# Kernel tuning notes

Measured on AMD Instinct MI355X. Metric: run time of the kernel, lower is better.

The kernel has to match this reference:

```python
import math
import jax, jax.numpy as jnp
import numpy as np

KERNEL_SIZES = [3, 5, 7, 9, 11, 13, 15, 17]
NUM_HEADS = 2
EMBED = len(KERNEL_SIZES)  # 8
HEAD_DIM = EMBED // NUM_HEADS  # 4


def _moving_avg(x2, k):
    # x2: [B, S]; replicate-pad so output length == S (MovingAvg padding scheme)
    front = k - 1 - (k - 1) // 2
    end = (k - 1) // 2
    p = jnp.concatenate([
        jnp.repeat(x2[:, :1], front, axis=1), x2,
        jnp.repeat(x2[:, -1:], end, axis=1)
    ], axis=1)  # [B, S+k-1]
    w = jnp.full((1, 1, k), 1.0 / k, dtype=x2.dtype)
    y = jax.lax.conv_general_dilated(p[:, None, :], w, (1,), 'VALID')
    return y[:, 0, :]  # [B, S]


def setup_inputs() -> dict:
    key = jax.random.key(0)
    ks = jax.random.split(key, 6)
    B, S = 32, 2048
    D, E = HEAD_DIM, EMBED
    sd = 1.0 / math.sqrt(D)
    x = jax.random.normal(ks[0], (B, S, 1), dtype=jnp.float32)
    Wq = jax.random.normal(ks[1], (D, D), dtype=jnp.float32) * sd
    Wk = jax.random.normal(ks[2], (D, D), dtype=jnp.float32) * sd
    Wv = jax.random.normal(ks[3], (D, D), dtype=jnp.float32) * sd
    Wo = jax.random.normal(ks[4], (E, E), dtype=jnp.float32) * (1.0 / math.sqrt(E))
    bo = jax.random.normal(ks[5], (E,), dtype=jnp.float32) * 0.01
    return {"x": x, "Wq": Wq, "Wk": Wk, "Wv": Wv, "Wo": Wo, "bo": bo}


def reference(x, Wq, Wk, Wv, Wo, bo):
    B, S, _ = x.shape
    H, D, E = NUM_HEADS, HEAD_DIM, EMBED
    x2 = x[..., 0]  # [B, S]
    # multi moving-average branches -> concat on channel dim
    mm = jnp.stack([_moving_avg(x2, k) for k in KERNEL_SIZES], axis=-1)  # [B,S,E]
    t = mm.reshape(B, S, H, D)
    # nn.Linear(head_dim, head_dim, bias=False): y = x @ W^T (shared across heads)
    q = jnp.einsum('bshd,ed->bshe', t, Wq)
    k_ = jnp.einsum('bshd,ed->bshe', t, Wk)
    v = jnp.einsum('bshd,ed->bshe', t, Wv)
    scale = jnp.asarray(math.sqrt(D), dtype=x.dtype)
    energy = jnp.einsum('bqhd,bkhd->bhqk', q, k_) / scale  # [B,H,S,S]
    att = jax.nn.softmax(energy, axis=-1)  # dropout is identity in eval mode
    o = jnp.einsum('bhqk,bkhd->bqhd', att, v).reshape(B, S, E)
    o = o @ Wo.T + bo  # fc_out
    weights = jax.nn.softmax(o, axis=-1)  # [B,S,E]
    trend = jnp.sum(mm * weights, axis=-1, keepdims=True)  # [B,S,1]
    seasonal = x - trend
    return seasonal, trend
```

## Files before the change

kernel.cpp:

```cpp
#include <hip/hip_runtime.h>

#define SB 32
#define SS 2048
#define SH 2
#define SD 4
#define SE 8

#define LOG2E 1.44269504f

typedef float    f32x16 __attribute__((ext_vector_type(16)));
typedef _Float16 f16x8  __attribute__((ext_vector_type(8)));

static __device__ __forceinline__ float fast_exp2(float x) {
#if __has_builtin(__builtin_amdgcn_exp2f)
    return __builtin_amdgcn_exp2f(x);
#else
    return exp2f(x);
#endif
}

static __device__ __forceinline__ int cvtpk(float a, float b) {
    auto h = __builtin_amdgcn_cvt_pkrtz(a, b);
    union { decltype(h) hh; int i; } u; u.hh = h; return u.i;
}

static __device__ __forceinline__ void swap32(int a, int b, int lane, int& r0, int& r1) {
#if __has_builtin(__builtin_amdgcn_permlane32_swap)
    auto r = __builtin_amdgcn_permlane32_swap(a, b, false, false);
    r0 = r[0]; r1 = r[1];
#else
    const int blo = __builtin_amdgcn_ds_bpermute((lane & 31) << 2, b);
    const int ahi = __builtin_amdgcn_ds_bpermute(((lane ^ 32) & 63) << 2, a);
    r0 = (lane < 32) ? a : blo;
    r1 = (lane < 32) ? ahi : b;
#endif
}

static __device__ __forceinline__ f16x8 frag2(unsigned x, unsigned y) {
    union { unsigned u[4]; f16x8 h; } c;
    c.u[0] = x; c.u[1] = y; c.u[2] = 0; c.u[3] = 0; return c.h;
}
static __device__ __forceinline__ f16x8 frag4(uint4 v) {
    union { uint4 u; f16x8 h; } c; c.u = v; return c.h;
}
static __device__ __forceinline__ f16x8 fragi(int a, int b, int c_, int d) {
    union { int u[4]; f16x8 h; } c;
    c.u[0] = a; c.u[1] = b; c.u[2] = c_; c.u[3] = d; return c.h;
}

union u32h2 { unsigned u; _Float16 h[2]; };
static __device__ __forceinline__ unsigned packh2(float a, float b) {
    u32h2 c; c.h[0] = (_Float16)a; c.h[1] = (_Float16)b; return c.u;
}

__global__ __launch_bounds__(256) void k_ma_qkv(
    const float* __restrict__ x,
    const float* __restrict__ Wq,
    const float* __restrict__ Wk,
    const float* __restrict__ Wv,
    uint2* __restrict__ qws16,
    uint2* __restrict__ kws16,
    _Float16* __restrict__ vtg,
    float4* __restrict__ mmws)
{
    __shared__ float xs[272];

    const int tile = blockIdx.x % (SS / 256);
    const int b    = blockIdx.x / (SS / 256);
    const int s0   = tile * 256;
    const float* xrow = x + b * SS;

    for (int i = threadIdx.x; i < 272; i += 256) {
        int idx = s0 - 8 + i;
        idx = min(max(idx, 0), SS - 1);
        xs[i] = xrow[idx];
    }
    __syncthreads();

    const int t = threadIdx.x;
    const int s = s0 + t;

    float mmv[8];
    float c = xs[8 + t];
    #pragma unroll
    for (int h = 1; h <= 8; ++h) {
        c += xs[8 + t - h] + xs[8 + t + h];
        mmv[h - 1] = c * (1.0f / (float)(2 * h + 1));
    }

    mmws[(b * SS + s) * 2 + 0] = make_float4(mmv[0], mmv[1], mmv[2], mmv[3]);
    mmws[(b * SS + s) * 2 + 1] = make_float4(mmv[4], mmv[5], mmv[6], mmv[7]);

    const float qscale = 0.5f * LOG2E;
    #pragma unroll
    for (int h = 0; h < SH; ++h) {
        const float t0 = mmv[h * 4 + 0];
        const float t1 = mmv[h * 4 + 1];
        const float t2 = mmv[h * 4 + 2];
        const float t3 = mmv[h * 4 + 3];
        float q[4], k[4], v[4];
        #pragma unroll
        for (int e = 0; e < 4; ++e) {
            q[e] = (t0 * Wq[e * 4 + 0] + t1 * Wq[e * 4 + 1] +
                    t2 * Wq[e * 4 + 2] + t3 * Wq[e * 4 + 3]) * qscale;
            k[e] =  t0 * Wk[e * 4 + 0] + t1 * Wk[e * 4 + 1] +
                    t2 * Wk[e * 4 + 2] + t3 * Wk[e * 4 + 3];
            v[e] =  t0 * Wv[e * 4 + 0] + t1 * Wv[e * 4 + 1] +
                    t2 * Wv[e * 4 + 2] + t3 * Wv[e * 4 + 3];
        }
        const int bh  = b * SH + h;
        const int idx = bh * SS + s;
        qws16[idx] = make_uint2(packh2(q[0], q[1]), packh2(q[2], q[3]));
        kws16[idx] = make_uint2(packh2(k[0], k[1]), packh2(k[2], k[3]));
        #pragma unroll
        for (int e = 0; e < 4; ++e)
            vtg[(bh * 4 + e) * SS + s] = (_Float16)v[e];
    }
}

#define LDS_K    0
#define LDS_VT   16384
#define VT_STRIDE 4112
#define LDS_Z    36944
#define LDS_SIZE 37376

__global__ __launch_bounds__(256) void k_attn(
    const uint2* __restrict__ qws16,
    const uint2* __restrict__ kws16,
    const unsigned* __restrict__ vtg,
    float4* __restrict__ ows)
{
    __shared__ __align__(16) char lds[LDS_SIZE];

    const int t      = threadIdx.x;
    const int bh     = blockIdx.x >> 4;
    const int w      = t >> 6;
    const int iblock = (blockIdx.x & 15) * 4 + w;
    const int lane   = t & 63;
    const int c31    = lane & 31;

    const uint2* kg = kws16 + bh * SS;
    for (int i = t; i < SS; i += 256)
        *(uint2*)(lds + LDS_K + i * 8) = kg[i];
    const unsigned* vg = vtg + bh * 4 * (SS / 2);
    for (int i = t; i < 4 * (SS / 2); i += 256) {
        const int cc = i >> 10, col = i & 1023;
        *(unsigned*)(lds + LDS_VT + cc * VT_STRIDE + col * 4) = vg[i];
    }
    for (int i = t; i < SS / 2; i += 256)
        *(unsigned*)(lds + LDS_VT + 4 * VT_STRIDE + i * 4) = 0x3C003C00u;
    if (t < 32) *(unsigned*)(lds + LDS_Z + t * 4) = 0u;
    __syncthreads();

    uint2 qq = qws16[bh * SS + iblock * 32 + c31];
    if (lane >= 32) { qq.x = 0u; qq.y = 0u; }
    const f16x8 bq = frag2(qq.x, qq.y);

    int kaddr = (lane < 32) ? (LDS_K + lane * 8) : LDS_Z;
    const int kstep = (lane < 32) ? 256 : 0;
    int vaddr = (c31 < 5) ? (LDS_VT + c31 * VT_STRIDE + (lane >> 5) * 16) : LDS_Z;
    const int vstep = (c31 < 5) ? 64 : 0;

    f32x16 oacc = {0,0,0,0,0,0,0,0,0,0,0,0,0,0,0,0};
    const f32x16 zc = {0,0,0,0,0,0,0,0,0,0,0,0,0,0,0,0};

    uint2 kk  = *(const uint2*)(lds + kaddr); kaddr += kstep;
    uint4 vv0 = *(const uint4*)(lds + vaddr);
    uint4 vv1 = *(const uint4*)(lds + vaddr + 32); vaddr += vstep;

    for (int jt = 0; jt < SS / 32; ++jt) {
        const f16x8 ak  = frag2(kk.x, kk.y);
        const f16x8 av0 = frag4(vv0);
        const f16x8 av1 = frag4(vv1);

        f32x16 d = __builtin_amdgcn_mfma_f32_32x32x16_f16(ak, bq, zc, 0, 0, 0);

        kk  = *(const uint2*)(lds + kaddr); kaddr += kstep;
        vv0 = *(const uint4*)(lds + vaddr);
        vv1 = *(const uint4*)(lds + vaddr + 32); vaddr += vstep;

        float p[16];
        #pragma unroll
        for (int r = 0; r < 16; ++r) p[r] = fast_exp2(d[r]);

        const int pk01 = cvtpk(p[0],  p[1]),  pk23 = cvtpk(p[2],  p[3]);
        const int pk45 = cvtpk(p[4],  p[5]),  pk67 = cvtpk(p[6],  p[7]);
        const int pk89 = cvtpk(p[8],  p[9]),  pkAB = cvtpk(p[10], p[11]);
        const int pkCD = cvtpk(p[12], p[13]), pkEF = cvtpk(p[14], p[15]);

        int B0, B1, B2, B3, C0, C1, C2, C3;
        swap32(pk01, pk45, lane, B0, B2);
        swap32(pk23, pk67, lane, B1, B3);
        swap32(pk89, pkCD, lane, C0, C2);
        swap32(pkAB, pkEF, lane, C1, C3);

        const f16x8 bp0 = fragi(B0, B1, B2, B3);
        const f16x8 bp1 = fragi(C0, C1, C2, C3);

        oacc = __builtin_amdgcn_mfma_f32_32x32x16_f16(av0, bp0, oacc, 0, 0, 0);
        oacc = __builtin_amdgcn_mfma_f32_32x32x16_f16(av1, bp1, oacc, 0, 0, 0);
    }

    union { float f; int i; } u0; u0.f = oacc[0];
    int s0i, s1i;
    swap32(u0.i, u0.i, lane, s0i, s1i);
    union { int i; float f; } ul; ul.i = s1i;
    if (lane < 32) {
        const float inv = 1.0f / ul.f;
        ows[bh * SS + iblock * 32 + lane] =
            make_float4(oacc[0] * inv, oacc[1] * inv, oacc[2] * inv, oacc[3] * inv);
    }
}

__global__ __launch_bounds__(256) void k_epilogue(
    const float* __restrict__ x,
    const float* __restrict__ Wo,
    const float* __restrict__ bo,
    const float4* __restrict__ ows,
    const float4* __restrict__ mmws,
    float* __restrict__ out)
{
    const int pos = blockIdx.x * 256 + threadIdx.x;
    const int b = pos / SS;
    const int s = pos % SS;

    const float4 o0 = ows[(b * SH + 0) * SS + s];
    const float4 o1 = ows[(b * SH + 1) * SS + s];
    const float ov[8] = {o0.x, o0.y, o0.z, o0.w, o1.x, o1.y, o1.z, o1.w};

    float g[8];
    float m = -1e30f;
    #pragma unroll
    for (int e = 0; e < 8; ++e) {
        float acc = bo[e];
        #pragma unroll
        for (int f = 0; f < 8; ++f) acc += ov[f] * Wo[e * 8 + f];
        g[e] = acc;
        m = fmaxf(m, acc);
    }
    float l = 0.0f;
    #pragma unroll
    for (int e = 0; e < 8; ++e) { g[e] = __expf(g[e] - m); l += g[e]; }
    const float inv = 1.0f / l;

    const float4 mm0 = mmws[pos * 2 + 0];
    const float4 mm1 = mmws[pos * 2 + 1];
    const float mv[8] = {mm0.x, mm0.y, mm0.z, mm0.w, mm1.x, mm1.y, mm1.z, mm1.w};

    float trend = 0.0f;
    #pragma unroll
    for (int e = 0; e < 8; ++e) trend += g[e] * inv * mv[e];

    out[pos]           = x[pos] - trend;
    out[SB * SS + pos] = trend;
}

extern "C" void kernel_launch(void* const* d_in, const int* in_sizes, int n_in,
                              void* d_out, int out_size, void* d_ws, size_t ws_size,
                              hipStream_t stream) {
    const float* x  = (const float*)d_in[0];
    const float* Wq = (const float*)d_in[1];
    const float* Wk = (const float*)d_in[2];
    const float* Wv = (const float*)d_in[3];
    const float* Wo = (const float*)d_in[4];
    const float* bo = (const float*)d_in[5];

    uint2*     qws16 = (uint2*)d_ws;
    uint2*     kws16 = qws16 + SB * SH * SS;
    _Float16*  vtg   = (_Float16*)(kws16 + SB * SH * SS);
    float4*    mmws  = (float4*)(vtg + SB * SH * 4 * SS);
    float4*    ows   = mmws + SB * SS * 2;

    k_ma_qkv<<<SB * (SS / 256), 256, 0, stream>>>(x, Wq, Wk, Wv, qws16, kws16, vtg, mmws);
    k_attn<<<SB * SH * 16, 256, 0, stream>>>(qws16, kws16, (const unsigned*)vtg, ows);
    k_epilogue<<<(SB * SS) / 256, 256, 0, stream>>>(x, Wo, bo, ows, mmws, (float*)d_out);
}
```

Baseline: 51.17 us.

## Split attention key dimension into two chunks and reduce partials in epilogue

The attention kernel now processes half of the key/value sequence per block, doubling the grid and halving LDS usage per block. Each block writes unnormalized partial outputs and partial row sums, and the epilogue kernel sums the chunks and normalizes. This aims to improve occupancy and CU utilization and shorten each block's serial loop. The cost is extra workspace traffic for partials and more reads in the epilogue.

```diff
diff --git a/kernel.cpp b/kernel.cpp
--- a/kernel.cpp
+++ b/kernel.cpp
@@ -5,6 +5,11 @@
 #define SH 2
 #define SD 4
 #define SE 8
+#define BHS (SB * SH * SS)
+
+#define JCH  2
+#define JLEN (SS / JCH)
+#define NT   (JLEN / 32)
 
 #define LOG2E 1.44269504f
 
@@ -118,36 +123,40 @@
     }
 }
 
-#define LDS_K    0
-#define LDS_VT   16384
-#define VT_STRIDE 4112
-#define LDS_Z    36944
-#define LDS_SIZE 37376
-
-__global__ __launch_bounds__(256) void k_attn(
+#define LDS_K     0
+#define K_BYTES   (JLEN * 8)
+#define LDS_VT    K_BYTES
+#define VT_STRIDE ((JLEN + 8) * 2)
+#define LDS_Z     (LDS_VT + 5 * VT_STRIDE)
+#define LDS_SIZE  (LDS_Z + 128)
+
+__global__ __launch_bounds__(256, 8) void k_attn(
     const uint2* __restrict__ qws16,
     const uint2* __restrict__ kws16,
     const unsigned* __restrict__ vtg,
-    float4* __restrict__ ows)
+    float4* __restrict__ pacc,
+    float* __restrict__ pl)
 {
     __shared__ __align__(16) char lds[LDS_SIZE];
 
-    const int t      = threadIdx.x;
-    const int bh     = blockIdx.x >> 4;
-    const int w      = t >> 6;
-    const int iblock = (blockIdx.x & 15) * 4 + w;
-    const int lane   = t & 63;
-    const int c31    = lane & 31;
-
-    const uint2* kg = kws16 + bh * SS;
-    for (int i = t; i < SS; i += 256)
+    const int t    = threadIdx.x;
+    const int jc   = blockIdx.x & (JCH - 1);
+    const int ig   = (blockIdx.x >> 1) & 15;
+    const int bh   = blockIdx.x >> 5;
+    const int w    = t >> 6;
+    const int iblock = ig * 4 + w;
+    const int lane = t & 63;
+    const int c31  = lane & 31;
+
+    const uint2* kg = kws16 + bh * SS + jc * JLEN;
+    for (int i = t; i < JLEN; i += 256)
         *(uint2*)(lds + LDS_K + i * 8) = kg[i];
-    const unsigned* vg = vtg + bh * 4 * (SS / 2);
-    for (int i = t; i < 4 * (SS / 2); i += 256) {
-        const int cc = i >> 10, col = i & 1023;
-        *(unsigned*)(lds + LDS_VT + cc * VT_STRIDE + col * 4) = vg[i];
-    }
-    for (int i = t; i < SS / 2; i += 256)
+    const unsigned* vg = vtg + bh * 4 * (SS / 2) + jc * (JLEN / 2);
+    for (int i = t; i < 4 * (JLEN / 2); i += 256) {
+        const int cc = i / (JLEN / 2), col = i % (JLEN / 2);
+        *(unsigned*)(lds + LDS_VT + cc * VT_STRIDE + col * 4) = vg[cc * (SS / 2) + col];
+    }
+    for (int i = t; i < JLEN / 2; i += 256)
         *(unsigned*)(lds + LDS_VT + 4 * VT_STRIDE + i * 4) = 0x3C003C00u;
     if (t < 32) *(unsigned*)(lds + LDS_Z + t * 4) = 0u;
     __syncthreads();
@@ -168,7 +177,7 @@
     uint4 vv0 = *(const uint4*)(lds + vaddr);
     uint4 vv1 = *(const uint4*)(lds + vaddr + 32); vaddr += vstep;
 
-    for (int jt = 0; jt < SS / 32; ++jt) {
+    for (int jt = 0; jt < NT; ++jt) {
         const f16x8 ak  = frag2(kk.x, kk.y);
         const f16x8 av0 = frag4(vv0);
         const f16x8 av1 = frag4(vv1);
@@ -206,9 +215,9 @@
     swap32(u0.i, u0.i, lane, s0i, s1i);
     union { int i; float f; } ul; ul.i = s1i;
     if (lane < 32) {
-        const float inv = 1.0f / ul.f;
-        ows[bh * SS + iblock * 32 + lane] =
-            make_float4(oacc[0] * inv, oacc[1] * inv, oacc[2] * inv, oacc[3] * inv);
+        const int idx = jc * BHS + bh * SS + iblock * 32 + lane;
+        pacc[idx] = make_float4(oacc[0], oacc[1], oacc[2], oacc[3]);
+        pl[idx]   = ul.f;
     }
 }
 
@@ -216,7 +225,8 @@
     const float* __restrict__ x,
     const float* __restrict__ Wo,
     const float* __restrict__ bo,
-    const float4* __restrict__ ows,
+    const float4* __restrict__ pacc,
+    const float* __restrict__ pl,
     const float4* __restrict__ mmws,
     float* __restrict__ out)
 {
@@ -224,9 +234,23 @@
     const int b = pos / SS;
     const int s = pos % SS;
 
-    const float4 o0 = ows[(b * SH + 0) * SS + s];
-    const float4 o1 = ows[(b * SH + 1) * SS + s];
-    const float ov[8] = {o0.x, o0.y, o0.z, o0.w, o1.x, o1.y, o1.z, o1.w};
+    float ov[8];
+    #pragma unroll
+    for (int h = 0; h < SH; ++h) {
+        const int base = (b * SH + h) * SS + s;
+        float lsum = 0.f, ax = 0.f, ay = 0.f, az = 0.f, aw = 0.f;
+        #pragma unroll
+        for (int jc = 0; jc < JCH; ++jc) {
+            const float4 pa = pacc[jc * BHS + base];
+            lsum += pl[jc * BHS + base];
+            ax += pa.x; ay += pa.y; az += pa.z; aw += pa.w;
+        }
+        const float inv = 1.0f / lsum;
+        ov[h * 4 + 0] = ax * inv;
+        ov[h * 4 + 1] = ay * inv;
+        ov[h * 4 + 2] = az * inv;
+        ov[h * 4 + 3] = aw * inv;
+    }
 
     float g[8];
     float m = -1e30f;
@@ -266,12 +290,13 @@
     const float* bo = (const float*)d_in[5];
 
     uint2*     qws16 = (uint2*)d_ws;
-    uint2*     kws16 = qws16 + SB * SH * SS;
-    _Float16*  vtg   = (_Float16*)(kws16 + SB * SH * SS);
-    float4*    mmws  = (float4*)(vtg + SB * SH * 4 * SS);
-    float4*    ows   = mmws + SB * SS * 2;
+    uint2*     kws16 = qws16 + BHS;
+    _Float16*  vtg   = (_Float16*)(kws16 + BHS);
+    float4*    mmws  = (float4*)(vtg + 4 * BHS);
+    float4*    pacc  = mmws + SB * SS * 2;
+    float*     pl    = (float*)(pacc + JCH * BHS);
 
     k_ma_qkv<<<SB * (SS / 256), 256, 0, stream>>>(x, Wq, Wk, Wv, qws16, kws16, vtg, mmws);
-    k_attn<<<SB * SH * 16, 256, 0, stream>>>(qws16, kws16, (const unsigned*)vtg, ows);
-    k_epilogue<<<(SB * SS) / 256, 256, 0, stream>>>(x, Wo, bo, ows, mmws, (float*)d_out);
-}
+    k_attn<<<SB * SH * 16 * JCH, 256, 0, stream>>>(qws16, kws16, (const unsigned*)vtg, pacc, pl);
+    k_epilogue<<<(SB * SS) / 256, 256, 0, stream>>>(x, Wo, bo, pacc, pl, mmws, (float*)d_out);
+}
```

Measured after the change: 56.52 us. 10.5% more time.

## Software-pipeline QK MFMA ahead of exp in attention loop with ping-pong tiles

Applied to the files above, without the earlier changes.

Restructures the attention inner loop into two interleaved stages (A/B). The QK^T MFMA for a later tile is issued before the exp/pack/PV work of the current tile, so MFMA latency overlaps with VALU exp and permute work. It also raises wave priority around the PV MFMAs with s_setprio and adds a min-blocks hint of 4 to launch bounds. The costs are more live registers for two score tiles, two wasted MFMAs and LDS over-reads at the tail, and a risk that the occupancy hint forces register spills.

```diff
diff --git a/kernel.cpp b/kernel.cpp
--- a/kernel.cpp
+++ b/kernel.cpp
@@ -123,8 +123,9 @@
 #define VT_STRIDE 4112
 #define LDS_Z    36944
 #define LDS_SIZE 37376
-
-__global__ __launch_bounds__(256) void k_attn(
+#define NT       (SS / 32)
+
+__global__ __launch_bounds__(256, 4) void k_attn(
     const uint2* __restrict__ qws16,
     const uint2* __restrict__ kws16,
     const unsigned* __restrict__ vtg,
@@ -164,41 +165,76 @@
     f32x16 oacc = {0,0,0,0,0,0,0,0,0,0,0,0,0,0,0,0};
     const f32x16 zc = {0,0,0,0,0,0,0,0,0,0,0,0,0,0,0,0};
 
-    uint2 kk  = *(const uint2*)(lds + kaddr); kaddr += kstep;
-    uint4 vv0 = *(const uint4*)(lds + vaddr);
-    uint4 vv1 = *(const uint4*)(lds + vaddr + 32); vaddr += vstep;
-
-    for (int jt = 0; jt < SS / 32; ++jt) {
-        const f16x8 ak  = frag2(kk.x, kk.y);
-        const f16x8 av0 = frag4(vv0);
-        const f16x8 av1 = frag4(vv1);
-
-        f32x16 d = __builtin_amdgcn_mfma_f32_32x32x16_f16(ak, bq, zc, 0, 0, 0);
-
-        kk  = *(const uint2*)(lds + kaddr); kaddr += kstep;
-        vv0 = *(const uint4*)(lds + vaddr);
-        vv1 = *(const uint4*)(lds + vaddr + 32); vaddr += vstep;
-
-        float p[16];
-        #pragma unroll
-        for (int r = 0; r < 16; ++r) p[r] = fast_exp2(d[r]);
-
-        const int pk01 = cvtpk(p[0],  p[1]),  pk23 = cvtpk(p[2],  p[3]);
-        const int pk45 = cvtpk(p[4],  p[5]),  pk67 = cvtpk(p[6],  p[7]);
-        const int pk89 = cvtpk(p[8],  p[9]),  pkAB = cvtpk(p[10], p[11]);
-        const int pkCD = cvtpk(p[12], p[13]), pkEF = cvtpk(p[14], p[15]);
-
-        int B0, B1, B2, B3, C0, C1, C2, C3;
-        swap32(pk01, pk45, lane, B0, B2);
-        swap32(pk23, pk67, lane, B1, B3);
-        swap32(pk89, pkCD, lane, C0, C2);
-        swap32(pkAB, pkEF, lane, C1, C3);
-
-        const f16x8 bp0 = fragi(B0, B1, B2, B3);
-        const f16x8 bp1 = fragi(C0, C1, C2, C3);
-
-        oacc = __builtin_amdgcn_mfma_f32_32x32x16_f16(av0, bp0, oacc, 0, 0, 0);
-        oacc = __builtin_amdgcn_mfma_f32_32x32x16_f16(av1, bp1, oacc, 0, 0, 0);
+    uint2 kkA = *(const uint2*)(lds + kaddr); kaddr += kstep;
+    uint2 kkB = *(const uint2*)(lds + kaddr); kaddr += kstep;
+    uint4 vvA0 = *(const uint4*)(lds + vaddr);
+    uint4 vvA1 = *(const uint4*)(lds + vaddr + 32); vaddr += vstep;
+    f32x16 dA = __builtin_amdgcn_mfma_f32_32x32x16_f16(frag2(kkA.x, kkA.y), bq, zc, 0, 0, 0);
+    kkA = *(const uint2*)(lds + kaddr); kaddr += kstep;
+    f32x16 dB = __builtin_amdgcn_mfma_f32_32x32x16_f16(frag2(kkB.x, kkB.y), bq, zc, 0, 0, 0);
+    kkB = *(const uint2*)(lds + kaddr); kaddr += kstep;
+    uint4 vvB0 = *(const uint4*)(lds + vaddr);
+    uint4 vvB1 = *(const uint4*)(lds + vaddr + 32); vaddr += vstep;
+
+    for (int jt = 0; jt < NT; jt += 2) {
+        {
+            float p[16];
+            #pragma unroll
+            for (int r = 0; r < 16; ++r) p[r] = fast_exp2(dA[r]);
+
+            dA = __builtin_amdgcn_mfma_f32_32x32x16_f16(frag2(kkA.x, kkA.y), bq, zc, 0, 0, 0);
+            kkA = *(const uint2*)(lds + kaddr); kaddr += kstep;
+
+            const f16x8 avA0 = frag4(vvA0);
+            const f16x8 avA1 = frag4(vvA1);
+            vvA0 = *(const uint4*)(lds + vaddr);
+            vvA1 = *(const uint4*)(lds + vaddr + 32); vaddr += vstep;
+
+            const int pk01 = cvtpk(p[0],  p[1]),  pk23 = cvtpk(p[2],  p[3]);
+            const int pk45 = cvtpk(p[4],  p[5]),  pk67 = cvtpk(p[6],  p[7]);
+            const int pk89 = cvtpk(p[8],  p[9]),  pkAB = cvtpk(p[10], p[11]);
+            const int pkCD = cvtpk(p[12], p[13]), pkEF = cvtpk(p[14], p[15]);
+
+            int B0, B1, B2, B3, C0, C1, C2, C3;
+            swap32(pk01, pk45, lane, B0, B2);
+            swap32(pk23, pk67, lane, B1, B3);
+            swap32(pk89, pkCD, lane, C0, C2);
+            swap32(pkAB, pkEF, lane, C1, C3);
+
+            __builtin_amdgcn_s_setprio(1);
+            oacc = __builtin_amdgcn_mfma_f32_32x32x16_f16(avA0, fragi(B0, B1, B2, B3), oacc, 0, 0, 0);
+            oacc = __builtin_amdgcn_mfma_f32_32x32x16_f16(avA1, fragi(C0, C1, C2, C3), oacc, 0, 0, 0);
+            __builtin_amdgcn_s_setprio(0);
+        }
+        {
+            float p[16];
+            #pragma unroll
+            for (int r = 0; r < 16; ++r) p[r] = fast_exp2(dB[r]);
+
+            dB = __builtin_amdgcn_mfma_f32_32x32x16_f16(frag2(kkB.x, kkB.y), bq, zc, 0, 0, 0);
+            kkB = *(const uint2*)(lds + kaddr); kaddr += kstep;
+
+            const f16x8 avB0 = frag4(vvB0);
+            const f16x8 avB1 = frag4(vvB1);
+            vvB0 = *(const uint4*)(lds + vaddr);
+            vvB1 = *(const uint4*)(lds + vaddr + 32); vaddr += vstep;
+
+            const int pk01 = cvtpk(p[0],  p[1]),  pk23 = cvtpk(p[2],  p[3]);
+            const int pk45 = cvtpk(p[4],  p[5]),  pk67 = cvtpk(p[6],  p[7]);
+            const int pk89 = cvtpk(p[8],  p[9]),  pkAB = cvtpk(p[10], p[11]);
+            const int pkCD = cvtpk(p[12], p[13]), pkEF = cvtpk(p[14], p[15]);
+
+            int B0, B1, B2, B3, C0, C1, C2, C3;
+            swap32(pk01, pk45, lane, B0, B2);
+            swap32(pk23, pk67, lane, B1, B3);
+            swap32(pk89, pkCD, lane, C0, C2);
+            swap32(pkAB, pkEF, lane, C1, C3);
+
+            __builtin_amdgcn_s_setprio(1);
+            oacc = __builtin_amdgcn_mfma_f32_32x32x16_f16(avB0, fragi(B0, B1, B2, B3), oacc, 0, 0, 0);
+            oacc = __builtin_amdgcn_mfma_f32_32x32x16_f16(avB1, fragi(C0, C1, C2, C3), oacc, 0, 0, 0);
+            __builtin_amdgcn_s_setprio(0);
+        }
     }
 
     union { float f; int i; } u0; u0.f = oacc[0];
```

Result: faster. 48.06 us (-6.1%).
